# Kernel optimization log

Hardware: AMD Instinct MI355X
Metric: run time of the kernel (lower is better)

The kernel has to match this reference:

```python
import jax, jax.numpy as jnp
import numpy as np

NUM_HEADS = 16

def setup_inputs() -> dict:
    key = jax.random.key(0)
    ks = jax.random.split(key, 6)
    B, S, D = 2, 2048, 1024
    return {
        "hidden_states": jax.random.normal(ks[0], (B, S, D), dtype=jnp.float32),
        "c_attn_w": jax.random.normal(ks[1], (D, 3 * D), dtype=jnp.float32) * 0.02,
        "c_attn_b": jax.random.normal(ks[2], (3 * D,), dtype=jnp.float32) * 0.02,
        "attn_bias": jax.random.normal(ks[3], (S, S), dtype=jnp.float32) * 0.02,
        "c_proj_w": jax.random.normal(ks[4], (D, D), dtype=jnp.float32) * 0.02,
        "c_proj_b": jax.random.normal(ks[5], (D,), dtype=jnp.float32) * 0.02,
    }

def reference(hidden_states, c_attn_w, c_attn_b, attn_bias, c_proj_w, c_proj_b):
    B, S, D = hidden_states.shape
    H = NUM_HEADS
    hd = D // H
    # fused QKV projection: [B,S,3D]
    qkv = hidden_states @ c_attn_w + c_attn_b
    q, k, v = jnp.split(qkv, 3, axis=-1)
    # [B,H,S,hd]
    q = q.reshape(B, S, H, hd).transpose(0, 2, 1, 3)
    k = k.reshape(B, S, H, hd).transpose(0, 2, 1, 3)
    v = v.reshape(B, S, H, hd).transpose(0, 2, 1, 3)
    # scores [B,H,S,S] with learned additive bias and causal mask
    scores = jnp.einsum('bhqd,bhkd->bhqk', q, k) / jnp.sqrt(jnp.float32(hd))
    scores = scores + attn_bias[:S, :S][None, None, :, :]
    causal = jnp.tril(jnp.ones((S, S), dtype=bool))
    scores = jnp.where(causal[None, None, :, :], scores, jnp.float32(-1e9))
    attn = jax.nn.softmax(scores, axis=-1)
    ctx = jnp.einsum('bhqk,bhkd->bhqd', attn, v)
    ctx = ctx.transpose(0, 2, 1, 3).reshape(B, S, D)
    out = ctx @ c_proj_w + c_proj_b  # resid dropout is identity in eval
    return (out, k, v)
```

## Files before the change

kernel.cpp:

```cpp
#include <hip/hip_runtime.h>
#include <hip/hip_bf16.h>
#include <stdint.h>


typedef __attribute__((ext_vector_type(4))) float f32x4;
typedef __attribute__((ext_vector_type(16))) float f32x16;
typedef __attribute__((ext_vector_type(8))) short s16x8;
typedef __attribute__((ext_vector_type(4))) short s16x4;
typedef unsigned short u16;

#define LOG2E 1.4426950408889634f
#define QSCALE 0.18033688011112042f

__device__ __forceinline__ u16 f2bf(float f) {
  unsigned w;
  asm("v_cvt_pk_bf16_f32 %0, %1, %2" : "=v"(w) : "v"(f), "v"(f));
  return (u16)w;
}
__device__ __forceinline__ unsigned cvtpk(float lo, float hi) {
  unsigned w;
  asm("v_cvt_pk_bf16_f32 %0, %1, %2" : "=v"(w) : "v"(lo), "v"(hi));
  return w;
}
__device__ __forceinline__ float bf2f(u16 h) {
  unsigned int x = ((unsigned int)h) << 16;
  return __builtin_bit_cast(float, x);
}
__device__ __forceinline__ float fexp2(float x) {
  float r;
  asm("v_exp_f32 %0, %1" : "=v"(r) : "v"(x));
  return r;
}
__device__ __forceinline__ void pl32swap(unsigned& a, unsigned& b) {
  asm volatile("v_permlane32_swap_b32 %0, %1" : "+v"(a), "+v"(b));
}
__device__ __forceinline__ s16x8 frag8(unsigned a, unsigned b, unsigned c, unsigned d) {
  union { unsigned u[4]; s16x8 v; } t;
  t.u[0] = a; t.u[1] = b; t.u[2] = c; t.u[3] = d;
  return t.v;
}
__device__ __forceinline__ f32x16 mfma32(s16x8 a, s16x8 b, f32x16 c) {
  return __builtin_amdgcn_mfma_f32_32x32x16_bf16(a, b, c, 0, 0, 0);
}

__device__ __forceinline__ void gload_lds16(const u16* g, u16* lds) {
  __builtin_amdgcn_global_load_lds(
      (const __attribute__((address_space(1))) unsigned int*)g,
      (__attribute__((address_space(3))) unsigned int*)lds, 16, 0, 0);
}


__global__ __launch_bounds__(256) void cvt_f32_bf16(const float* __restrict__ x,
                                                    u16* __restrict__ y, int n4) {
  int i = blockIdx.x * 256 + threadIdx.x;
  if (i < n4) {
    f32x4 v = *(const f32x4*)&x[(size_t)i * 4];
    s16x4 o;
    o[0] = (short)f2bf(v[0]); o[1] = (short)f2bf(v[1]);
    o[2] = (short)f2bf(v[2]); o[3] = (short)f2bf(v[3]);
    *(s16x4*)&y[(size_t)i * 4] = o;
  }
}

__global__ __launch_bounds__(256) void transpose_w_bf16(const float* __restrict__ W,
                                                        u16* __restrict__ WT,
                                                        int K, int N) {
  __shared__ float tile[32][33];
  const int n0 = blockIdx.x * 32, k0 = blockIdx.y * 32;
  const int tx = threadIdx.x & 31, ty = threadIdx.x >> 5;
#pragma unroll
  for (int i = 0; i < 32; i += 8)
    tile[ty + i][tx] = W[(size_t)(k0 + ty + i) * N + (n0 + tx)];
  __syncthreads();
#pragma unroll
  for (int i = 0; i < 32; i += 8)
    WT[(size_t)(n0 + ty + i) * K + (k0 + tx)] = f2bf(tile[tx][ty + i]);
}

__global__ __launch_bounds__(128) void bias_tile(const float* __restrict__ B,
                                                 u16* __restrict__ T) {
  const int kt = blockIdx.x;
  const int q32 = blockIdx.y;
  if (kt > (q32 >> 1)) return;
  const int t = threadIdx.x >> 6, lane = threadIdx.x & 63;
  const int hh = q32 >> 1;
  const size_t boff = (size_t)(hh + (q32 & 1)) * (hh + 1);
  const int q = q32 * 32 + (lane & 31);
  const int kb = kt * 64 + t * 32 + 4 * (lane >> 5);
  u16 v[16];
#pragma unroll
  for (int r = 0; r < 16; r++) {
    const int k = kb + (r & 3) + 8 * (r >> 2);
    v[r] = (k <= q) ? f2bf(B[(size_t)q * 2048 + k] * LOG2E) : (u16)0xFF80;
  }
  u16* dst = T + (boff + kt) * 2048 + t * 1024 + (size_t)lane * 16;
  *(s16x8*)dst = *(s16x8*)&v[0];
  *(s16x8*)(dst + 8) = *(s16x8*)&v[8];
}


template <int MODE>
__global__ __launch_bounds__(256) void gemm_bt(
    const u16* __restrict__ A, const u16* __restrict__ BT,
    const float* __restrict__ bias, float* __restrict__ outF,
    u16* __restrict__ q_ws, u16* __restrict__ k_ws, u16* __restrict__ vT_ws,
    int M, int N, int K) {
  __shared__ u16 As[128 * 32];
  __shared__ u16 Bs[128 * 32];
  const int nwg = gridDim.x * gridDim.y;
  int flat = blockIdx.y * gridDim.x + blockIdx.x;
  flat = (flat & 7) * (nwg >> 3) + (flat >> 3);
  const int m0 = (flat / gridDim.x) * 128, n0 = (flat % gridDim.x) * 128;
  const int tid = threadIdx.x;
  const int wid = tid >> 6, lane = tid & 63;
  const int c = lane & 15, hi = lane >> 4;
  const int wm = wid >> 1, wn = wid & 1;
  const int srow = lane >> 2;
  const int skp = (lane & 3) * 8;

  f32x4 acc[4][4] = {};

  for (int k0 = 0; k0 < K; k0 += 32) {
#pragma unroll
    for (int t = 0; t < 2; t++) {
      const int rowl = wid * 32 + t * 16;
      gload_lds16(&A[(size_t)(m0 + rowl + srow) * K + k0 + skp], &As[rowl * 32]);
      gload_lds16(&BT[(size_t)(n0 + rowl + srow) * K + k0 + skp], &Bs[rowl * 32]);
    }
    __syncthreads();
    s16x8 af[4], bfr[4];
#pragma unroll
    for (int i = 0; i < 4; i++)
      af[i] = *(const s16x8*)&As[(wm * 64 + i * 16 + c) * 32 + hi * 8];
#pragma unroll
    for (int i = 0; i < 4; i++)
      bfr[i] = *(const s16x8*)&Bs[(wn * 64 + i * 16 + c) * 32 + hi * 8];
#pragma unroll
    for (int i = 0; i < 4; i++)
#pragma unroll
      for (int j = 0; j < 4; j++)
        acc[i][j] = __builtin_amdgcn_mfma_f32_16x16x32_bf16(af[i], bfr[j], acc[i][j], 0, 0, 0);
    __syncthreads();
  }

#pragma unroll
  for (int i = 0; i < 4; i++) {
#pragma unroll
    for (int j = 0; j < 4; j++) {
      const int col = n0 + wn * 64 + j * 16 + c;
      const int rb = m0 + wm * 64 + i * 16 + hi * 4;
      const float bv = bias[col];
      if (MODE == 1) {
#pragma unroll
        for (int u = 0; u < 4; u++)
          outF[(size_t)(rb + u) * N + col] = acc[i][j][u] + bv;
      } else {
        const int which = col >> 10;
        const int h = (col >> 6) & 15, d = col & 63;
#pragma unroll
        for (int u = 0; u < 4; u++) {
          const int r = rb + u;
          const int b = r >> 11, s = r & 2047;
          const size_t idx = (size_t)(b * 16 + h) * 131072u + (size_t)s * 64 + d;
          const float v = acc[i][j][u] + bv;
          if (which == 0) {
            q_ws[idx] = f2bf(v * QSCALE);
          } else if (which == 1) {
            outF[4194304u + idx] = v;
            k_ws[idx] = f2bf(v);
          } else {
            outF[8388608u + idx] = v;
            vT_ws[(size_t)(b * 16 + h) * 131072u + (size_t)d * 2048 + s] = f2bf(v);
          }
        }
      }
    }
  }
}


__global__ __launch_bounds__(256, 4) void attn_fused(
    const u16* __restrict__ q_ws, const u16* __restrict__ k_ws,
    const u16* __restrict__ vT_ws, const u16* __restrict__ biasT,
    u16* __restrict__ ctx) {
  __shared__ u16 Ks[2][64 * 64];
  __shared__ u16 Vs[2][64 * 64];

  const int id = blockIdx.x;
  const int bh = (id & 7) * 4 + ((id >> 3) & 3);
  const int j = id >> 5, j0 = j & 7, sg = j >> 3;
  const int qblk = (sg == 0) ? j0 : (sg == 1) ? (15 - j0)
                 : (sg == 2) ? (16 + j0) : (31 - j0);

  const int wid = threadIdx.x >> 6, lane = threadIdx.x & 63;
  const int pq = wid >> 1, par = wid & 1;
  const int l31 = lane & 31, hi5 = lane >> 5;
  const int qrow0 = qblk * 64 + pq * 32;

  const u16* qh = q_ws + (size_t)bh * 131072u;
  const u16* kh = k_ws + (size_t)bh * 131072u;
  const u16* vh = vT_ws + (size_t)bh * 131072u;

  s16x8 qf[4];
#pragma unroll
  for (int s = 0; s < 4; s++)
    qf[s] = *(const s16x8*)&qh[(size_t)(qrow0 + l31) * 64 + s * 16 + hi5 * 8];

  const int q32 = qblk * 2 + pq;
  const int hh = q32 >> 1;
  const size_t boff = (size_t)(hh + (q32 & 1)) * (hh + 1);
  const u16* bbase = biasT + boff * 2048 + (size_t)par * 1024 + (size_t)lane * 16;

  const int sl_r = lane >> 3, sl_c = lane & 7;

  f32x16 o0 = {}, o1 = {};
  float mrow = -1e30f, lpart = 0.f;

#define STAGE(BUF, N0)                                                        \
  {                                                                           \
    _Pragma("unroll")                                                         \
    for (int t = 0; t < 2; t++) {                                             \
      const int rb = wid * 16 + t * 8;                                        \
      const int r = rb + sl_r;                                                \
      gload_lds16(&kh[(size_t)((N0) + r) * 64 + ((sl_c ^ (r & 7)) * 8)],      \
                  &Ks[BUF][rb * 64]);                                         \
      gload_lds16(&vh[(size_t)r * 2048 + (N0) + ((sl_c ^ (r & 7)) * 8)],      \
                  &Vs[BUF][rb * 64]);                                         \
    }                                                                         \
  }

  STAGE(0, 0);
  __syncthreads();

  int buf = 0;
  const int nkt = qblk + 1;
  const int swz = l31 & 7;
  const int arow = par * 32 + l31;

  s16x8 bc0 = *(const s16x8*)(bbase);
  s16x8 bc1 = *(const s16x8*)(bbase + 8);

  for (int kt = 0; kt < nkt; ++kt) {
    if (kt + 1 < nkt) {
      if (buf) { STAGE(0, kt * 64 + 64); } else { STAGE(1, kt * 64 + 64); }
    }
    const u16* btn = bbase + (size_t)((kt + 1 < nkt) ? kt + 1 : kt) * 2048;
    const s16x8 bn0 = *(const s16x8*)(btn);
    const s16x8 bn1 = *(const s16x8*)(btn + 8);

    f32x16 s0;
#pragma unroll
    for (int r = 0; r < 8; r++) {
      s0[r] = bf2f((u16)bc0[r]);
      s0[r + 8] = bf2f((u16)bc1[r]);
    }

    const u16* ksb = &Ks[buf][0];
    __builtin_amdgcn_s_setprio(1);
#pragma unroll
    for (int s = 0; s < 4; s++) {
      const int ch = ((s * 2 + hi5) ^ swz) * 8;
      const s16x8 a0 = *(const s16x8*)&ksb[arow * 64 + ch];
      s0 = mfma32(a0, qf[s], s0);
    }
    __builtin_amdgcn_s_setprio(0);

    float t0 = fmaxf(fmaxf(s0[0], s0[1]), fmaxf(s0[2], s0[3]));
    float t1 = fmaxf(fmaxf(s0[4], s0[5]), fmaxf(s0[6], s0[7]));
    float t2 = fmaxf(fmaxf(s0[8], s0[9]), fmaxf(s0[10], s0[11]));
    float t3 = fmaxf(fmaxf(s0[12], s0[13]), fmaxf(s0[14], s0[15]));
    float tm = fmaxf(fmaxf(t0, t1), fmaxf(t2, t3));
    tm = fmaxf(tm, __shfl_xor(tm, 32));

    if (__any(tm > mrow + 8.f)) {
      const float nm = fmaxf(mrow, tm);
      const float al = fexp2(mrow - nm);
      mrow = nm;
      lpart *= al;
#pragma unroll
      for (int r = 0; r < 16; r++) { o0[r] *= al; o1[r] *= al; }
    }

    float a0s = 0.f, a1s = 0.f;
#pragma unroll
    for (int r = 0; r < 8; r++) {
      s0[r] = fexp2(s0[r] - mrow);       a0s += s0[r];
      s0[r + 8] = fexp2(s0[r + 8] - mrow); a1s += s0[r + 8];
    }
    lpart += a0s + a1s;

    unsigned wv0 = cvtpk(s0[0], s0[1]),   wv1 = cvtpk(s0[2], s0[3]);
    unsigned wv2 = cvtpk(s0[4], s0[5]),   wv3 = cvtpk(s0[6], s0[7]);
    unsigned wv4 = cvtpk(s0[8], s0[9]),   wv5 = cvtpk(s0[10], s0[11]);
    unsigned wv6 = cvtpk(s0[12], s0[13]), wv7 = cvtpk(s0[14], s0[15]);
    pl32swap(wv0, wv2); pl32swap(wv1, wv3);
    pl32swap(wv4, wv6); pl32swap(wv5, wv7);

    const u16* vsb = &Vs[buf][0];
    __builtin_amdgcn_s_setprio(1);
#pragma unroll
    for (int hf = 0; hf < 2; hf++) {
      const s16x8 pa = hf ? frag8(wv4, wv5, wv6, wv7) : frag8(wv0, wv1, wv2, wv3);
      const int s = par * 2 + hf;
      const int ch = ((s * 2 + hi5) ^ swz) * 8;
      const s16x8 v0 = *(const s16x8*)&vsb[l31 * 64 + ch];
      const s16x8 v1 = *(const s16x8*)&vsb[(32 + l31) * 64 + ch];
      o0 = mfma32(pa, v0, o0);
      o1 = mfma32(pa, v1, o1);
    }
    __builtin_amdgcn_s_setprio(0);

    __syncthreads();
    buf ^= 1;
    bc0 = bn0; bc1 = bn1;
  }
#undef STAGE

  lpart += __shfl_xor(lpart, 32);

  float* obuf = (float*)&Ks[0][0];
  float2* mlb = (float2*)&Vs[0][0];

  __syncthreads();
  if (hi5 == 0) mlb[(par * 2 + pq) * 64 + l31] = make_float2(mrow, lpart);
  if (par == 1) {
    const int slot = pq * 64 + lane;
#pragma unroll
    for (int r = 0; r < 16; r++) {
      obuf[r * 128 + slot] = o0[r];
      obuf[(16 + r) * 128 + slot] = o1[r];
    }
  }
  __syncthreads();
  if (par == 0) {
    const int slot = pq * 64 + lane;
    const int b = bh >> 4, h = bh & 15;
#pragma unroll
    for (int r = 0; r < 16; r++) {
      const int qloc = (r & 3) + 8 * (r >> 2) + 4 * hi5;
      const float2 Aml = mlb[pq * 64 + qloc];
      const float2 Bml = mlb[(2 + pq) * 64 + qloc];
      const float mm = fmaxf(Aml.x, Bml.x);
      const float fa = fexp2(Aml.x - mm), fb = fexp2(Bml.x - mm);
      const float inv = __builtin_amdgcn_rcpf(Aml.y * fa + Bml.y * fb);
      const float om0 = (o0[r] * fa + obuf[r * 128 + slot] * fb) * inv;
      const float om1 = (o1[r] * fa + obuf[(16 + r) * 128 + slot] * fb) * inv;
      const int tok = b * 2048 + qrow0 + qloc;
      ctx[(size_t)tok * 1024 + h * 64 + l31] = f2bf(om0);
      ctx[(size_t)tok * 1024 + h * 64 + 32 + l31] = f2bf(om1);
    }
  }
}


extern "C" void kernel_launch(void* const* d_in, const int* in_sizes, int n_in,
                              void* d_out, int out_size, void* d_ws, size_t ws_size,
                              hipStream_t stream) {
  const float* hs        = (const float*)d_in[0];
  const float* c_attn_w  = (const float*)d_in[1];
  const float* c_attn_b  = (const float*)d_in[2];
  const float* attn_bias = (const float*)d_in[3];
  const float* c_proj_w  = (const float*)d_in[4];
  const float* c_proj_b  = (const float*)d_in[5];
  float* out = (float*)d_out;

  uint8_t* ws = (uint8_t*)d_ws;
  u16* hsb    = (u16*)(ws + 0);
  u16* wqkvT  = (u16*)(ws + 8388608u);
  u16* wprojT = (u16*)(ws + 14680064u);
  u16* q_ws   = (u16*)(ws + 16777216u);
  u16* k_ws   = (u16*)(ws + 25165824u);
  u16* vT_ws  = (u16*)(ws + 33554432u);
  u16* ctx    = (u16*)(ws + 41943040u);
  u16* biasT  = hsb;

  cvt_f32_bf16<<<4096, 256, 0, stream>>>(hs, hsb, 1048576);
  transpose_w_bf16<<<dim3(96, 32), 256, 0, stream>>>(c_attn_w, wqkvT, 1024, 3072);
  transpose_w_bf16<<<dim3(32, 32), 256, 0, stream>>>(c_proj_w, wprojT, 1024, 1024);

  gemm_bt<0><<<dim3(24, 32), 256, 0, stream>>>(hsb, wqkvT, c_attn_b, out,
                                               q_ws, k_ws, vT_ws, 4096, 3072, 1024);

  bias_tile<<<dim3(32, 64), 128, 0, stream>>>(attn_bias, biasT);

  attn_fused<<<dim3(1024), 256, 0, stream>>>(q_ws, k_ws, vT_ws, biasT, ctx);

  gemm_bt<1><<<dim3(8, 32), 256, 0, stream>>>(ctx, wprojT, c_proj_b, out,
                                              (u16*)nullptr, (u16*)nullptr, (u16*)nullptr,
                                              4096, 1024, 1024);
}
```

Baseline: 143.0 us.

## Replace QKV GEMM with 256x256-tile double-buffered direct-to-LDS kernel

```diff
diff --git a/kernel.cpp b/kernel.cpp
--- a/kernel.cpp
+++ b/kernel.cpp
@@ -99,11 +99,115 @@
 }
 
 
-template <int MODE>
+__global__ __launch_bounds__(512, 2) void gemm_qkv8(
+    const u16* __restrict__ A, const u16* __restrict__ BT,
+    const float* __restrict__ bias, float* __restrict__ outF,
+    u16* __restrict__ q_ws, u16* __restrict__ k_ws, u16* __restrict__ vT_ws) {
+  __shared__ u16 As[2][256 * 64];
+  __shared__ u16 Bs[2][256 * 64];
+
+  const int flat0 = blockIdx.y * 12 + blockIdx.x;
+  const int flat = (flat0 & 7) * 24 + (flat0 >> 3);
+  const int m0 = (flat / 12) * 256;
+  const int n0 = (flat % 12) * 256;
+
+  const int tid = threadIdx.x;
+  const int wid = tid >> 6, lane = tid & 63;
+  const int c16 = lane & 15, hi4 = lane >> 4;
+  const int wm = wid >> 2, wn = wid & 3;
+  const int srow8 = lane >> 3;
+  const int ch = (lane & 7) ^ srow8;
+
+  f32x4 acc[8][4] = {};
+
+#define STG8(SLOT, KT)                                                        \
+  {                                                                           \
+    _Pragma("unroll")                                                         \
+    for (int n = 0; n < 4; n++) {                                             \
+      const int r = wid * 32 + n * 8;                                         \
+      gload_lds16(&A[(size_t)(m0 + r + srow8) * 1024 + (KT) * 64 + ch * 8],   \
+                  &As[SLOT][r * 64]);                                         \
+    }                                                                         \
+    _Pragma("unroll")                                                         \
+    for (int n = 0; n < 4; n++) {                                             \
+      const int r = wid * 32 + n * 8;                                         \
+      gload_lds16(&BT[(size_t)(n0 + r + srow8) * 1024 + (KT) * 64 + ch * 8],  \
+                  &Bs[SLOT][r * 64]);                                         \
+    }                                                                         \
+  }
+
+  STG8(0, 0);
+  STG8(1, 1);
+
+  for (int t = 0; t < 16; ++t) {
+    if (t < 15) { asm volatile("s_waitcnt vmcnt(8)" ::: "memory"); }
+    else        { asm volatile("s_waitcnt vmcnt(0)" ::: "memory"); }
+    __builtin_amdgcn_s_barrier();
+    asm volatile("" ::: "memory");
+
+    const int cur = t & 1;
+#pragma unroll
+    for (int ks = 0; ks < 2; ks++) {
+      s16x8 af[8], bfr[4];
+#pragma unroll
+      for (int i = 0; i < 8; i++) {
+        const int r = wm * 128 + i * 16 + c16;
+        af[i] = *(const s16x8*)&As[cur][r * 64 + (((ks * 4 + hi4) ^ (c16 & 7)) * 8)];
+      }
+#pragma unroll
+      for (int j = 0; j < 4; j++) {
+        const int r = wn * 64 + j * 16 + c16;
+        bfr[j] = *(const s16x8*)&Bs[cur][r * 64 + (((ks * 4 + hi4) ^ (c16 & 7)) * 8)];
+      }
+      __builtin_amdgcn_s_setprio(1);
+#pragma unroll
+      for (int i = 0; i < 8; i++)
+#pragma unroll
+        for (int j = 0; j < 4; j++)
+          acc[i][j] = __builtin_amdgcn_mfma_f32_16x16x32_bf16(af[i], bfr[j], acc[i][j], 0, 0, 0);
+      __builtin_amdgcn_s_setprio(0);
+    }
+
+    asm volatile("" ::: "memory");
+    __builtin_amdgcn_s_barrier();
+    asm volatile("" ::: "memory");
+    if (t + 2 < 16) { STG8(cur, t + 2); }
+  }
+#undef STG8
+
+#pragma unroll
+  for (int i = 0; i < 8; i++) {
+#pragma unroll
+    for (int j = 0; j < 4; j++) {
+      const int col = n0 + wn * 64 + j * 16 + c16;
+      const int rb = m0 + wm * 128 + i * 16 + hi4 * 4;
+      const float bv = bias[col];
+      const int which = col >> 10;
+      const int h = (col >> 6) & 15, d = col & 63;
+#pragma unroll
+      for (int u = 0; u < 4; u++) {
+        const int r = rb + u;
+        const int b = r >> 11, s = r & 2047;
+        const size_t idx = (size_t)(b * 16 + h) * 131072u + (size_t)s * 64 + d;
+        const float v = acc[i][j][u] + bv;
+        if (which == 0) {
+          q_ws[idx] = f2bf(v * QSCALE);
+        } else if (which == 1) {
+          outF[4194304u + idx] = v;
+          k_ws[idx] = f2bf(v);
+        } else {
+          outF[8388608u + idx] = v;
+          vT_ws[(size_t)(b * 16 + h) * 131072u + (size_t)d * 2048 + s] = f2bf(v);
+        }
+      }
+    }
+  }
+}
+
+
 __global__ __launch_bounds__(256) void gemm_bt(
     const u16* __restrict__ A, const u16* __restrict__ BT,
     const float* __restrict__ bias, float* __restrict__ outF,
-    u16* __restrict__ q_ws, u16* __restrict__ k_ws, u16* __restrict__ vT_ws,
     int M, int N, int K) {
   __shared__ u16 As[128 * 32];
   __shared__ u16 Bs[128 * 32];
@@ -150,30 +254,9 @@
       const int col = n0 + wn * 64 + j * 16 + c;
       const int rb = m0 + wm * 64 + i * 16 + hi * 4;
       const float bv = bias[col];
-      if (MODE == 1) {
-#pragma unroll
-        for (int u = 0; u < 4; u++)
-          outF[(size_t)(rb + u) * N + col] = acc[i][j][u] + bv;
-      } else {
-        const int which = col >> 10;
-        const int h = (col >> 6) & 15, d = col & 63;
-#pragma unroll
-        for (int u = 0; u < 4; u++) {
-          const int r = rb + u;
-          const int b = r >> 11, s = r & 2047;
-          const size_t idx = (size_t)(b * 16 + h) * 131072u + (size_t)s * 64 + d;
-          const float v = acc[i][j][u] + bv;
-          if (which == 0) {
-            q_ws[idx] = f2bf(v * QSCALE);
-          } else if (which == 1) {
-            outF[4194304u + idx] = v;
-            k_ws[idx] = f2bf(v);
-          } else {
-            outF[8388608u + idx] = v;
-            vT_ws[(size_t)(b * 16 + h) * 131072u + (size_t)d * 2048 + s] = f2bf(v);
-          }
-        }
-      }
+#pragma unroll
+      for (int u = 0; u < 4; u++)
+        outF[(size_t)(rb + u) * N + col] = acc[i][j][u] + bv;
     }
   }
 }
@@ -259,8 +342,8 @@
     __builtin_amdgcn_s_setprio(1);
 #pragma unroll
     for (int s = 0; s < 4; s++) {
-      const int ch = ((s * 2 + hi5) ^ swz) * 8;
-      const s16x8 a0 = *(const s16x8*)&ksb[arow * 64 + ch];
+      const int chq = ((s * 2 + hi5) ^ swz) * 8;
+      const s16x8 a0 = *(const s16x8*)&ksb[arow * 64 + chq];
       s0 = mfma32(a0, qf[s], s0);
     }
     __builtin_amdgcn_s_setprio(0);
@@ -302,9 +385,9 @@
     for (int hf = 0; hf < 2; hf++) {
       const s16x8 pa = hf ? frag8(wv4, wv5, wv6, wv7) : frag8(wv0, wv1, wv2, wv3);
       const int s = par * 2 + hf;
-      const int ch = ((s * 2 + hi5) ^ swz) * 8;
-      const s16x8 v0 = *(const s16x8*)&vsb[l31 * 64 + ch];
-      const s16x8 v1 = *(const s16x8*)&vsb[(32 + l31) * 64 + ch];
+      const int chv = ((s * 2 + hi5) ^ swz) * 8;
+      const s16x8 v0 = *(const s16x8*)&vsb[l31 * 64 + chv];
+      const s16x8 v1 = *(const s16x8*)&vsb[(32 + l31) * 64 + chv];
       o0 = mfma32(pa, v0, o0);
       o1 = mfma32(pa, v1, o1);
     }
@@ -378,14 +461,13 @@
   transpose_w_bf16<<<dim3(96, 32), 256, 0, stream>>>(c_attn_w, wqkvT, 1024, 3072);
   transpose_w_bf16<<<dim3(32, 32), 256, 0, stream>>>(c_proj_w, wprojT, 1024, 1024);
 
-  gemm_bt<0><<<dim3(24, 32), 256, 0, stream>>>(hsb, wqkvT, c_attn_b, out,
-                                               q_ws, k_ws, vT_ws, 4096, 3072, 1024);
+  gemm_qkv8<<<dim3(12, 16), 512, 0, stream>>>(hsb, wqkvT, c_attn_b, out,
+                                              q_ws, k_ws, vT_ws);
 
   bias_tile<<<dim3(32, 64), 128, 0, stream>>>(attn_bias, biasT);
 
   attn_fused<<<dim3(1024), 256, 0, stream>>>(q_ws, k_ws, vT_ws, biasT, ctx);
 
-  gemm_bt<1><<<dim3(8, 32), 256, 0, stream>>>(ctx, wprojT, c_proj_b, out,
-                                              (u16*)nullptr, (u16*)nullptr, (u16*)nullptr,
-                                              4096, 1024, 1024);
-}
+  gemm_bt<<<dim3(8, 32), 256, 0, stream>>>(ctx, wprojT, c_proj_b, out,
+                                           4096, 1024, 1024);
+}
```

Result: slower. 159.5 us (+11.5%).

## Double-buffer GEMM LDS tiles and move V transpose into a separate kernel

Applied to the files above, without the earlier changes.

```diff
diff --git a/kernel.cpp b/kernel.cpp
--- a/kernel.cpp
+++ b/kernel.cpp
@@ -75,6 +75,24 @@
 #pragma unroll
   for (int i = 0; i < 32; i += 8)
     WT[(size_t)(n0 + ty + i) * K + (k0 + tx)] = f2bf(tile[tx][ty + i]);
+}
+
+__global__ __launch_bounds__(256) void transpose_v(const u16* __restrict__ v,
+                                                   u16* __restrict__ vT) {
+  __shared__ u16 tile[64][72];
+  const int bh = blockIdx.y;
+  const int s0 = blockIdx.x * 64;
+  const int tr = threadIdx.x >> 2, tc = (threadIdx.x & 3) * 16;
+  const u16* src = v + (size_t)bh * 131072u + (size_t)(s0 + tr) * 64 + tc;
+  *(s16x8*)&tile[tr][tc] = *(const s16x8*)src;
+  *(s16x8*)&tile[tr][tc + 8] = *(const s16x8*)(src + 8);
+  __syncthreads();
+  u16 o[16];
+#pragma unroll
+  for (int x = 0; x < 16; x++) o[x] = tile[tc + x][tr];
+  u16* dst = vT + (size_t)bh * 131072u + (size_t)tr * 2048 + s0 + tc;
+  *(s16x8*)dst = *(s16x8*)&o[0];
+  *(s16x8*)(dst + 8) = *(s16x8*)&o[8];
 }
 
 __global__ __launch_bounds__(128) void bias_tile(const float* __restrict__ B,
@@ -103,10 +121,10 @@
 __global__ __launch_bounds__(256) void gemm_bt(
     const u16* __restrict__ A, const u16* __restrict__ BT,
     const float* __restrict__ bias, float* __restrict__ outF,
-    u16* __restrict__ q_ws, u16* __restrict__ k_ws, u16* __restrict__ vT_ws,
+    u16* __restrict__ q_ws, u16* __restrict__ k_ws, u16* __restrict__ v_ws,
     int M, int N, int K) {
-  __shared__ u16 As[128 * 32];
-  __shared__ u16 Bs[128 * 32];
+  __shared__ u16 As[2][128 * 32];
+  __shared__ u16 Bs[2][128 * 32];
   const int nwg = gridDim.x * gridDim.y;
   int flat = blockIdx.y * gridDim.x + blockIdx.x;
   flat = (flat & 7) * (nwg >> 3) + (flat >> 3);
@@ -120,42 +138,67 @@
 
   f32x4 acc[4][4] = {};
 
+#define STG(SLOT, K0)                                                         \
+  {                                                                           \
+    _Pragma("unroll")                                                         \
+    for (int t = 0; t < 2; t++) {                                             \
+      const int rowl = wid * 32 + t * 16;                                     \
+      gload_lds16(&A[(size_t)(m0 + rowl + srow) * K + (K0) + skp],            \
+                  &As[SLOT][rowl * 32]);                                      \
+      gload_lds16(&BT[(size_t)(n0 + rowl + srow) * K + (K0) + skp],           \
+                  &Bs[SLOT][rowl * 32]);                                      \
+    }                                                                         \
+  }
+
+  STG(0, 0);
+  __syncthreads();
+
+  int bufi = 0;
   for (int k0 = 0; k0 < K; k0 += 32) {
-#pragma unroll
-    for (int t = 0; t < 2; t++) {
-      const int rowl = wid * 32 + t * 16;
-      gload_lds16(&A[(size_t)(m0 + rowl + srow) * K + k0 + skp], &As[rowl * 32]);
-      gload_lds16(&BT[(size_t)(n0 + rowl + srow) * K + k0 + skp], &Bs[rowl * 32]);
-    }
-    __syncthreads();
+    if (k0 + 32 < K) {
+      if (bufi) { STG(0, k0 + 32); } else { STG(1, k0 + 32); }
+    }
     s16x8 af[4], bfr[4];
 #pragma unroll
     for (int i = 0; i < 4; i++)
-      af[i] = *(const s16x8*)&As[(wm * 64 + i * 16 + c) * 32 + hi * 8];
+      af[i] = *(const s16x8*)&As[bufi][(wm * 64 + i * 16 + c) * 32 + hi * 8];
 #pragma unroll
     for (int i = 0; i < 4; i++)
-      bfr[i] = *(const s16x8*)&Bs[(wn * 64 + i * 16 + c) * 32 + hi * 8];
+      bfr[i] = *(const s16x8*)&Bs[bufi][(wn * 64 + i * 16 + c) * 32 + hi * 8];
+    __builtin_amdgcn_s_setprio(1);
 #pragma unroll
     for (int i = 0; i < 4; i++)
 #pragma unroll
       for (int j = 0; j < 4; j++)
         acc[i][j] = __builtin_amdgcn_mfma_f32_16x16x32_bf16(af[i], bfr[j], acc[i][j], 0, 0, 0);
+    __builtin_amdgcn_s_setprio(0);
     __syncthreads();
-  }
-
-#pragma unroll
-  for (int i = 0; i < 4; i++) {
-#pragma unroll
-    for (int j = 0; j < 4; j++) {
-      const int col = n0 + wn * 64 + j * 16 + c;
-      const int rb = m0 + wm * 64 + i * 16 + hi * 4;
-      const float bv = bias[col];
-      if (MODE == 1) {
+    bufi ^= 1;
+  }
+#undef STG
+
+  if (MODE == 1) {
+#pragma unroll
+    for (int i = 0; i < 4; i++) {
+#pragma unroll
+      for (int j = 0; j < 4; j++) {
+        const int col = n0 + wn * 64 + j * 16 + c;
+        const int rb = m0 + wm * 64 + i * 16 + hi * 4;
+        const float bv = bias[col];
 #pragma unroll
         for (int u = 0; u < 4; u++)
           outF[(size_t)(rb + u) * N + col] = acc[i][j][u] + bv;
-      } else {
-        const int which = col >> 10;
+      }
+    }
+  } else {
+    const int which = n0 >> 10;
+#pragma unroll
+    for (int i = 0; i < 4; i++) {
+#pragma unroll
+      for (int j = 0; j < 4; j++) {
+        const int col = n0 + wn * 64 + j * 16 + c;
+        const int rb = m0 + wm * 64 + i * 16 + hi * 4;
+        const float bv = bias[col];
         const int h = (col >> 6) & 15, d = col & 63;
 #pragma unroll
         for (int u = 0; u < 4; u++) {
@@ -170,7 +213,7 @@
             k_ws[idx] = f2bf(v);
           } else {
             outF[8388608u + idx] = v;
-            vT_ws[(size_t)(b * 16 + h) * 131072u + (size_t)d * 2048 + s] = f2bf(v);
+            v_ws[idx] = f2bf(v);
           }
         }
       }
@@ -259,8 +302,8 @@
     __builtin_amdgcn_s_setprio(1);
 #pragma unroll
     for (int s = 0; s < 4; s++) {
-      const int ch = ((s * 2 + hi5) ^ swz) * 8;
-      const s16x8 a0 = *(const s16x8*)&ksb[arow * 64 + ch];
+      const int chq = ((s * 2 + hi5) ^ swz) * 8;
+      const s16x8 a0 = *(const s16x8*)&ksb[arow * 64 + chq];
       s0 = mfma32(a0, qf[s], s0);
     }
     __builtin_amdgcn_s_setprio(0);
@@ -302,9 +345,9 @@
     for (int hf = 0; hf < 2; hf++) {
       const s16x8 pa = hf ? frag8(wv4, wv5, wv6, wv7) : frag8(wv0, wv1, wv2, wv3);
       const int s = par * 2 + hf;
-      const int ch = ((s * 2 + hi5) ^ swz) * 8;
-      const s16x8 v0 = *(const s16x8*)&vsb[l31 * 64 + ch];
-      const s16x8 v1 = *(const s16x8*)&vsb[(32 + l31) * 64 + ch];
+      const int chv = ((s * 2 + hi5) ^ swz) * 8;
+      const s16x8 v0 = *(const s16x8*)&vsb[l31 * 64 + chv];
+      const s16x8 v1 = *(const s16x8*)&vsb[(32 + l31) * 64 + chv];
       o0 = mfma32(pa, v0, o0);
       o1 = mfma32(pa, v1, o1);
     }
@@ -372,6 +415,7 @@
   u16* k_ws   = (u16*)(ws + 25165824u);
   u16* vT_ws  = (u16*)(ws + 33554432u);
   u16* ctx    = (u16*)(ws + 41943040u);
+  u16* v_ws   = ctx;
   u16* biasT  = hsb;
 
   cvt_f32_bf16<<<4096, 256, 0, stream>>>(hs, hsb, 1048576);
@@ -379,7 +423,9 @@
   transpose_w_bf16<<<dim3(32, 32), 256, 0, stream>>>(c_proj_w, wprojT, 1024, 1024);
 
   gemm_bt<0><<<dim3(24, 32), 256, 0, stream>>>(hsb, wqkvT, c_attn_b, out,
-                                               q_ws, k_ws, vT_ws, 4096, 3072, 1024);
+                                               q_ws, k_ws, v_ws, 4096, 3072, 1024);
+
+  transpose_v<<<dim3(32, 32), 256, 0, stream>>>(v_ws, vT_ws);
 
   bias_tile<<<dim3(32, 64), 128, 0, stream>>>(attn_bias, biasT);
 
```

New measurement: 132.9 us. -7.1%, faster.
